# Optimization experiments

Hardware: AMD Instinct MI355X
Metric: run time of the kernel (lower is better)

The kernel has to match this reference:

```python
import jax, jax.numpy as jnp
import numpy as np
from jax import lax

B, T_IN, T_AR = 512, 200, 200
H = 128
L = 2    # num_layers


def setup_inputs() -> dict:
    key = jax.random.key(0)
    k = jax.random.split(key, 8)
    s = 1.0 / np.sqrt(H)
    x = jax.random.normal(k[0], (B, T_IN, H), jnp.float32)
    lengths_in = jax.random.randint(k[1], (B,), T_IN // 2, T_IN + 1).astype(jnp.int32).at[0].set(T_IN)
    lengths_aureg = jax.random.randint(k[2], (B,), T_AR // 2, T_AR + 1).astype(jnp.int32).at[0].set(T_AR)
    mask_aureg = jnp.arange(T_AR)[None, :] < lengths_aureg[:, None]  # [B, T_ar] prefix mask
    W_ih = jax.random.uniform(k[3], (L, 4 * H, H), jnp.float32, -s, s)
    W_hh = jax.random.uniform(k[4], (L, 4 * H, H), jnp.float32, -s, s)
    b_ih = jax.random.uniform(k[5], (L, 4 * H), jnp.float32, -s, s)
    b_hh = jax.random.uniform(k[6], (L, 4 * H), jnp.float32, -s, s)
    return {"x": x, "lengths_in": lengths_in, "lengths_aureg": lengths_aureg,
            "mask_aureg": mask_aureg, "W_ih": W_ih, "W_hh": W_hh, "b_ih": b_ih, "b_hh": b_hh}


def _forward(x, lengths_in, mask_aureg, W_ih, W_hh, b_ih, b_hh):
    def cell_stack(x_t, h, c):
        # one LSTM time step through all layers. x_t: [B,H]; h,c: [L,B,H]
        inp = x_t
        hs, cs = [], []
        for l in range(L):
            z = inp @ W_ih[l].T + h[l] @ W_hh[l].T + (b_ih[l] + b_hh[l])
            i, f, g, o = jnp.split(z, 4, axis=-1)  # PyTorch gate order i,f,g,o
            c_new = jax.nn.sigmoid(f) * c[l] + jax.nn.sigmoid(i) * jnp.tanh(g)
            h_new = jax.nn.sigmoid(o) * jnp.tanh(c_new)
            hs.append(h_new)
            cs.append(c_new)
            inp = h_new
        return jnp.stack(hs), jnp.stack(cs)

    T_in = x.shape[1]
    mask_in = jnp.arange(T_in)[None, :] < lengths_in[:, None]  # [B, T_in]
    h0 = jnp.zeros((L, B, H), x.dtype)

    # Teacher-forcing pass == packed-sequence LSTM: states only advance where t < length,
    # padded output positions are zero (as pad_packed_sequence produces).
    def tf_step(carry, xs):
        h, c = carry
        x_t, m_t = xs  # [B,H], [B]
        h_new, c_new = cell_stack(x_t, h, c)
        m3 = m_t[None, :, None]
        h = jnp.where(m3, h_new, h)
        c = jnp.where(m3, c_new, c)
        out = jnp.where(m_t[:, None], h_new[-1], 0.0)
        return (h, c), out

    (h, c), outs_tf = lax.scan(tf_step, (h0, h0), (x.transpose(1, 0, 2), mask_in.T))
    outputs_teafo = outs_tf.transpose(1, 0, 2)  # [B, T_in, H]

    # input_aureg_init: last-layer hidden at each sequence's final real step
    x_init = h[-1]  # [B, H]

    def ar_step(carry, m_t):
        h, c, xp = carry
        h_new, c_new = cell_stack(xp, h, c)
        m3 = m_t[None, :, None]
        h = jnp.where(m3, h_new, h)
        c = jnp.where(m3, c_new, c)
        out = jnp.where(m_t[:, None], h_new[-1], 0.0)  # temp_output (zeros for inactive rows)
        return (h, c, out), out

    _, outs_ar = lax.scan(ar_step, (h, c, x_init), mask_aureg.T)
    outputs_aureg = outs_ar.transpose(1, 0, 2)  # [B, T_ar, H]
    return outputs_teafo, outputs_aureg


def reference(x, lengths_in, lengths_aureg, mask_aureg, W_ih, W_hh, b_ih, b_hh):
    return _forward(x, lengths_in, mask_aureg, W_ih, W_hh, b_ih, b_hh)
```

## Files before the change

kernel.cpp:

```cpp
#include <hip/hip_runtime.h>
#include <hip/hip_fp16.h>

typedef _Float16 half8 __attribute__((ext_vector_type(8)));
typedef _Float16 half4v __attribute__((ext_vector_type(4)));
typedef float f32x4 __attribute__((ext_vector_type(4)));

#define T_INS 200

constexpr int WI0O = 0;
constexpr int H0O  = 131072;
constexpr int H1O  = 139264;
constexpr int XTO  = 147456;
constexpr int BIO  = 155648;
constexpr int SMSZ = 159744;

constexpr size_t WSZ_PACK = 524288;

#define OFF(b, k) (((((b) << 8) | ((k) << 1))) ^ (((b) & 7) << 4))

#define BARRIER() asm volatile("s_waitcnt lgkmcnt(0)\n\ts_barrier" ::: "memory")

__device__ __forceinline__ float sigm(float x) {
  return __builtin_amdgcn_rcpf(1.0f + __builtin_amdgcn_exp2f(-1.44269504f * x));
}
__device__ __forceinline__ float tanh_f(float x) {
  return 1.0f - 2.0f * __builtin_amdgcn_rcpf(1.0f + __builtin_amdgcn_exp2f(2.88539008f * x));
}
__device__ __forceinline__ half8 cvt_frag(const float* __restrict__ src) {
  f32x4 a = *(const f32x4*)src;
  f32x4 b = *(const f32x4*)(src + 4);
  half8 h;
  h[0] = (_Float16)a[0]; h[1] = (_Float16)a[1]; h[2] = (_Float16)a[2]; h[3] = (_Float16)a[3];
  h[4] = (_Float16)b[0]; h[5] = (_Float16)b[1]; h[6] = (_Float16)b[2]; h[7] = (_Float16)b[3];
  return h;
}
__device__ __forceinline__ half8 cvt_frag_s(const float* __restrict__ src, float s) {
  f32x4 a = *(const f32x4*)src;
  f32x4 b = *(const f32x4*)(src + 4);
  half8 h;
  h[0] = (_Float16)(s * a[0]); h[1] = (_Float16)(s * a[1]);
  h[2] = (_Float16)(s * a[2]); h[3] = (_Float16)(s * a[3]);
  h[4] = (_Float16)(s * b[0]); h[5] = (_Float16)(s * b[1]);
  h[6] = (_Float16)(s * b[2]); h[7] = (_Float16)(s * b[3]);
  return h;
}
__device__ __forceinline__ int perm_row8(int w, int mt, int r) {
  return (r & 3) * 128 + w * 16 + (r >> 2) * 4 + mt;
}

template <int SCALED>
__device__ __forceinline__ float gates(const f32x4 a, float& c, bool mk) {
  float si, sf, tg, so;
  if (SCALED) {
    si = __builtin_amdgcn_rcpf(1.0f + __builtin_amdgcn_exp2f(a[0]));
    sf = __builtin_amdgcn_rcpf(1.0f + __builtin_amdgcn_exp2f(a[1]));
    tg = 1.0f - 2.0f * __builtin_amdgcn_rcpf(1.0f + __builtin_amdgcn_exp2f(a[2]));
    so = __builtin_amdgcn_rcpf(1.0f + __builtin_amdgcn_exp2f(a[3]));
  } else {
    si = sigm(a[0]); sf = sigm(a[1]); tg = tanh_f(a[2]); so = sigm(a[3]);
  }
  float cn = sf * c + si * tg;
  float hn = so * tanh_f(cn);
  c = mk ? cn : c;
  return hn;
}

__global__ __launch_bounds__(256) void pack_kernel(const float* __restrict__ W_ih,
                                                   const float* __restrict__ W_hh,
                                                   char* __restrict__ ws) {
  int gid = blockIdx.x * 256 + threadIdx.x;
  int G = gid >> 6, lane = gid & 63;
  int region = G >> 7, F = G & 127;
  int w = F >> 4, mt = (F >> 2) & 3, kf = F & 3;
  int r = lane & 15;
  int row = perm_row8(w, mt, r);
  int k0 = kf * 32 + (lane >> 4) * 8;
  float s = ((r & 3) == 2) ? 2.88539008f : -1.44269504f;
  const float* src;
  if (region == 0)      src = W_ih + (size_t)(512 + row) * 128 + k0;
  else if (region == 3) src = W_ih + (size_t)row * 128 + k0;
  else                  src = W_hh + (size_t)((region - 1) * 512 + row) * 128 + k0;
  *(half8*)(ws + (size_t)G * 1024 + lane * 16) = cvt_frag_s(src, s);
}

template <int PACKED>
__global__ __launch_bounds__(512, 2) void lstm_kernel(
    const float* __restrict__ x, const int* __restrict__ len_in,
    const int* __restrict__ len_ar, const float* __restrict__ W_ih,
    const float* __restrict__ W_hh, const float* __restrict__ b_ih,
    const float* __restrict__ b_hh, const char* __restrict__ ws,
    float* __restrict__ out) {
  __shared__ __attribute__((aligned(16))) char sm[SMSZ];
  float* biasS = (float*)(sm + BIO);

  const int tid = threadIdx.x;
  const int w = tid >> 6, lane = tid & 63;
  const int lb = lane & 15, lg = lane >> 4;
  const int k0b = lg * 8;
  const int u0 = w * 16 + lg * 4;
  const int batch = blockIdx.x * 16 + lb;
  const int Lin = len_in[batch];
  const int Lar = len_ar[batch];

  if (PACKED) {
    for (int j = 0; j < 16; ++j) {
      int pos = j * 8192 + tid * 16;
      *(half8*)(sm + WI0O + pos) = *(const half8*)(ws + 393216 + pos);
    }
  } else {
    for (int j = 0; j < 16; ++j) {
      int pos = tid * 256 + j * 16;
      int F = pos >> 10, ln = (pos >> 4) & 63;
      int fw = F >> 4, fmt = (F >> 2) & 3, fkf = F & 3;
      int row = perm_row8(fw, fmt, ln & 15);
      int k0 = fkf * 32 + (ln >> 4) * 8;
      *(half8*)(sm + WI0O + pos) = cvt_frag(W_ih + (size_t)row * 128 + k0);
    }
  }
  for (int i = tid; i < 1024; i += 512) {
    int l = i >> 9, rp = i & 511, u = rp >> 2, q = rp & 3;
    float s = PACKED ? ((q == 2) ? 2.88539008f : -1.44269504f) : 1.0f;
    biasS[i] = s * (b_ih[l * 512 + q * 128 + u] + b_hh[l * 512 + q * 128 + u]);
  }
#pragma unroll
  for (int i = 0; i < 2; ++i)
    *(f32x4*)(sm + H0O + tid * 16 + i * 8192) = (f32x4){0.f, 0.f, 0.f, 0.f};
  const int xb = tid >> 5, xk4 = (tid & 31) * 4;
  {
    f32x4 v = *(const f32x4*)(x + ((size_t)(blockIdx.x * 16 + xb) * T_INS) * 128 + xk4);
    half4v hx;
    hx[0] = (_Float16)v[0]; hx[1] = (_Float16)v[1];
    hx[2] = (_Float16)v[2]; hx[3] = (_Float16)v[3];
    *(half4v*)(sm + XTO + OFF(xb, xk4)) = hx;
  }

  half8 whh0[4][4], whh1[4][4], wi1[4][4];
  if (PACKED) {
    const char* base = ws + (size_t)lane * 16;
#pragma unroll
    for (int mt = 0; mt < 4; ++mt)
#pragma unroll
      for (int kf = 0; kf < 4; ++kf) {
        int fo = (w * 16 + mt * 4 + kf) * 1024;
        wi1[mt][kf]  = *(const half8*)(base + fo);
        whh0[mt][kf] = *(const half8*)(base + 131072 + fo);
        whh1[mt][kf] = *(const half8*)(base + 262144 + fo);
      }
  } else {
#pragma unroll
    for (int mt = 0; mt < 4; ++mt)
#pragma unroll
      for (int kf = 0; kf < 4; ++kf) {
        int row = perm_row8(w, mt, lb);
        wi1[mt][kf]  = cvt_frag(W_ih + (size_t)(512 + row) * 128 + kf * 32 + k0b);
        whh0[mt][kf] = cvt_frag(W_hh + (size_t)row * 128 + kf * 32 + k0b);
        whh1[mt][kf] = cvt_frag(W_hh + (size_t)(512 + row) * 128 + kf * 32 + k0b);
      }
  }

  float c0[4], c1[4];
  half4v hp0v, hp1v;
#pragma unroll
  for (int i = 0; i < 4; ++i) {
    c0[i] = c1[i] = 0.f;
    hp0v[i] = (_Float16)0.f; hp1v[i] = (_Float16)0.f;
  }
  __syncthreads();

  const float* xptr = x + ((size_t)(blockIdx.x * 16 + xb) * T_INS + 1) * 128 + xk4;
  float* optr = out + (size_t)batch * 25600 + u0;
  const size_t obase_ar = 13107200ull + (size_t)batch * 25600 + u0;
  const char* wi0base = sm + WI0O + w * 16384 + lane * 16;

  for (int t = 0; t < 400; ++t) {
    const int p = t & 1;
    const bool doX = (t < 199);
    f32x4 xpre = (f32x4){0.f, 0.f, 0.f, 0.f};
    if (doX) { xpre = *(const f32x4*)xptr; xptr += 128; }
    const bool mk = (t < 200) ? (t < Lin) : ((t - 200) < Lar);

    f32x4 acc[4];
    {
      const char* sX = (t < 200) ? (sm + XTO + p * 4096) : (sm + H1O + p * 4096);
      const char* sH = sm + H0O + (p ^ 1) * 4096;
      half8 bf[4];
#pragma unroll
      for (int mt = 0; mt < 4; ++mt)
        acc[mt] = *(const f32x4*)(biasS + (u0 + mt) * 4);
#pragma unroll
      for (int kf = 0; kf < 4; ++kf)
        bf[kf] = *(const half8*)(sH + OFF(lb, kf * 32 + k0b));
#pragma unroll
      for (int kf = 0; kf < 4; ++kf)
#pragma unroll
        for (int mt = 0; mt < 4; ++mt)
          acc[mt] = __builtin_amdgcn_mfma_f32_16x16x32_f16(whh0[mt][kf], bf[kf],
                                                           acc[mt], 0, 0, 0);
#pragma unroll
      for (int kf = 0; kf < 4; ++kf)
        bf[kf] = *(const half8*)(sX + OFF(lb, kf * 32 + k0b));
#pragma unroll
      for (int kf = 0; kf < 4; ++kf)
#pragma unroll
        for (int mt = 0; mt < 4; ++mt) {
          half8 a = *(const half8*)(wi0base + (mt * 4 + kf) * 1024);
          acc[mt] = __builtin_amdgcn_mfma_f32_16x16x32_f16(a, bf[kf], acc[mt], 0, 0, 0);
        }
    }
    {
      _Float16 h4[4];
#pragma unroll
      for (int mt = 0; mt < 4; ++mt)
        h4[mt] = (_Float16)gates<PACKED>(acc[mt], c0[mt], mk);
      hp0v = mk ? *(half4v*)h4 : hp0v;
      *(half4v*)(sm + H0O + p * 4096 + OFF(lb, u0)) = hp0v;
    }
    BARRIER();

    if (doX) {
      half4v hx;
      hx[0] = (_Float16)xpre[0]; hx[1] = (_Float16)xpre[1];
      hx[2] = (_Float16)xpre[2]; hx[3] = (_Float16)xpre[3];
      *(half4v*)(sm + XTO + (p ^ 1) * 4096 + OFF(xb, xk4)) = hx;
    }

    {
      const char* sX = sm + H0O + p * 4096;
      const char* sH = sm + H1O + p * 4096;
      half8 bf[4];
#pragma unroll
      for (int mt = 0; mt < 4; ++mt)
        acc[mt] = *(const f32x4*)(biasS + 512 + (u0 + mt) * 4);
#pragma unroll
      for (int kf = 0; kf < 4; ++kf)
        bf[kf] = *(const half8*)(sH + OFF(lb, kf * 32 + k0b));
#pragma unroll
      for (int kf = 0; kf < 4; ++kf)
#pragma unroll
        for (int mt = 0; mt < 4; ++mt)
          acc[mt] = __builtin_amdgcn_mfma_f32_16x16x32_f16(whh1[mt][kf], bf[kf],
                                                           acc[mt], 0, 0, 0);
#pragma unroll
      for (int kf = 0; kf < 4; ++kf)
        bf[kf] = *(const half8*)(sX + OFF(lb, kf * 32 + k0b));
#pragma unroll
      for (int kf = 0; kf < 4; ++kf)
#pragma unroll
        for (int mt = 0; mt < 4; ++mt)
          acc[mt] = __builtin_amdgcn_mfma_f32_16x16x32_f16(wi1[mt][kf], bf[kf],
                                                           acc[mt], 0, 0, 0);
    }
    {
      _Float16 h4[4];
      f32x4 vo;
#pragma unroll
      for (int mt = 0; mt < 4; ++mt) {
        float hn = gates<PACKED>(acc[mt], c1[mt], mk);
        h4[mt] = (_Float16)hn;
        vo[mt] = mk ? hn : 0.0f;
      }
      hp1v = mk ? *(half4v*)h4 : hp1v;
      *(half4v*)(sm + H1O + (p ^ 1) * 4096 + OFF(lb, u0)) = hp1v;
      *(f32x4*)optr = vo;
      optr += 128;
      if (t == 199) optr = out + obase_ar;
    }
    BARRIER();
  }
}

extern "C" void kernel_launch(void* const* d_in, const int* in_sizes, int n_in,
                              void* d_out, int out_size, void* d_ws, size_t ws_size,
                              hipStream_t stream) {
  (void)in_sizes; (void)n_in; (void)out_size;
  const float* x = (const float*)d_in[0];
  const int* len_in = (const int*)d_in[1];
  const int* len_ar = (const int*)d_in[2];
  const float* W_ih = (const float*)d_in[4];
  const float* W_hh = (const float*)d_in[5];
  const float* b_ih = (const float*)d_in[6];
  const float* b_hh = (const float*)d_in[7];
  float* out = (float*)d_out;
  char* ws = (char*)d_ws;

  if (ws_size >= WSZ_PACK) {
    pack_kernel<<<dim3(128), dim3(256), 0, stream>>>(W_ih, W_hh, ws);
    lstm_kernel<1><<<dim3(32), dim3(512), 0, stream>>>(x, len_in, len_ar, W_ih,
                                                       W_hh, b_ih, b_hh, ws, out);
  } else {
    lstm_kernel<0><<<dim3(32), dim3(512), 0, stream>>>(x, len_in, len_ar, W_ih,
                                                       W_hh, b_ih, b_hh, ws, out);
  }
}
```

Measured before the change: 1.052 ms.

## Split LSTM time loop into phases, prefetch recurrent operands across barriers, keep bias in registers

Splits the 400-step loop into separate teacher-forcing and autoregressive loops, which removes per-step branches on the phase. The recurrent-hidden fragments for the next matmul are now loaded before the barrier (software prefetch), and the barrier waits only for enough LDS ops to retire. Biases move from shared memory into registers and serve as the first MFMA accumulator input. This raises register pressure under the 512-thread, 2-block launch bounds, and the partial lgkmcnt wait must be correct for LDS ordering.

After: 1.604 ms. +52.5%, slower.

```diff
diff --git a/kernel.cpp b/kernel.cpp
--- a/kernel.cpp
+++ b/kernel.cpp
@@ -11,14 +11,13 @@
 constexpr int H0O  = 131072;
 constexpr int H1O  = 139264;
 constexpr int XTO  = 147456;
-constexpr int BIO  = 155648;
-constexpr int SMSZ = 159744;
+constexpr int SMSZ = 155648;
 
 constexpr size_t WSZ_PACK = 524288;
 
 #define OFF(b, k) (((((b) << 8) | ((k) << 1))) ^ (((b) & 7) << 4))
 
-#define BARRIER() asm volatile("s_waitcnt lgkmcnt(0)\n\ts_barrier" ::: "memory")
+#define BAR_K(n) asm volatile("s_waitcnt lgkmcnt(" #n ")\n\ts_barrier" ::: "memory")
 
 __device__ __forceinline__ float sigm(float x) {
   return __builtin_amdgcn_rcpf(1.0f + __builtin_amdgcn_exp2f(-1.44269504f * x));
@@ -83,6 +82,32 @@
   *(half8*)(ws + (size_t)G * 1024 + lane * 16) = cvt_frag_s(src, s);
 }
 
+#define READ_BF(BF, BASE)                                                     \
+  _Pragma("unroll") for (int kf = 0; kf < 4; ++kf)                            \
+      BF[kf] = *(const half8*)((BASE) + OFF(lb, kf * 32 + k0b));
+
+#define MFMA_H(ACC, WREG, BF, BIAS)                                           \
+  _Pragma("unroll") for (int mt = 0; mt < 4; ++mt)                            \
+      ACC[mt] = __builtin_amdgcn_mfma_f32_16x16x32_f16(WREG[mt][0], BF[0],    \
+                                                       BIAS[mt], 0, 0, 0);    \
+  _Pragma("unroll") for (int kf = 1; kf < 4; ++kf)                            \
+      _Pragma("unroll") for (int mt = 0; mt < 4; ++mt)                        \
+          ACC[mt] = __builtin_amdgcn_mfma_f32_16x16x32_f16(WREG[mt][kf],      \
+                                                           BF[kf], ACC[mt], 0, 0, 0);
+
+#define MFMA_X(ACC, WREG, BF)                                                 \
+  _Pragma("unroll") for (int kf = 0; kf < 4; ++kf)                            \
+      _Pragma("unroll") for (int mt = 0; mt < 4; ++mt)                        \
+          ACC[mt] = __builtin_amdgcn_mfma_f32_16x16x32_f16(WREG[mt][kf],      \
+                                                           BF[kf], ACC[mt], 0, 0, 0);
+
+#define MFMA_WI0(ACC, BF)                                                     \
+  _Pragma("unroll") for (int kf = 0; kf < 4; ++kf)                            \
+      _Pragma("unroll") for (int mt = 0; mt < 4; ++mt) {                      \
+        half8 a_ = *(const half8*)(wi0base + (mt * 4 + kf) * 1024);           \
+        ACC[mt] = __builtin_amdgcn_mfma_f32_16x16x32_f16(a_, BF[kf], ACC[mt], 0, 0, 0); \
+      }
+
 template <int PACKED>
 __global__ __launch_bounds__(512, 2) void lstm_kernel(
     const float* __restrict__ x, const int* __restrict__ len_in,
@@ -91,7 +116,6 @@
     const float* __restrict__ b_hh, const char* __restrict__ ws,
     float* __restrict__ out) {
   __shared__ __attribute__((aligned(16))) char sm[SMSZ];
-  float* biasS = (float*)(sm + BIO);
 
   const int tid = threadIdx.x;
   const int w = tid >> 6, lane = tid & 63;
@@ -116,11 +140,6 @@
       int k0 = fkf * 32 + (ln >> 4) * 8;
       *(half8*)(sm + WI0O + pos) = cvt_frag(W_ih + (size_t)row * 128 + k0);
     }
-  }
-  for (int i = tid; i < 1024; i += 512) {
-    int l = i >> 9, rp = i & 511, u = rp >> 2, q = rp & 3;
-    float s = PACKED ? ((q == 2) ? 2.88539008f : -1.44269504f) : 1.0f;
-    biasS[i] = s * (b_ih[l * 512 + q * 128 + u] + b_hh[l * 512 + q * 128 + u]);
   }
 #pragma unroll
   for (int i = 0; i < 2; ++i)
@@ -134,6 +153,18 @@
     *(half4v*)(sm + XTO + OFF(xb, xk4)) = hx;
   }
 
+  f32x4 bias0[4], bias1[4];
+#pragma unroll
+  for (int mt = 0; mt < 4; ++mt) {
+    int u = u0 + mt;
+#pragma unroll
+    for (int q = 0; q < 4; ++q) {
+      float s = PACKED ? ((q == 2) ? 2.88539008f : -1.44269504f) : 1.0f;
+      bias0[mt][q] = s * (b_ih[q * 128 + u] + b_hh[q * 128 + u]);
+      bias1[mt][q] = s * (b_ih[512 + q * 128 + u] + b_hh[512 + q * 128 + u]);
+    }
+  }
+
   half8 whh0[4][4], whh1[4][4], wi1[4][4];
   if (PACKED) {
     const char* base = ws + (size_t)lane * 16;
@@ -167,46 +198,25 @@
   }
   __syncthreads();
 
+  const char* wi0base = sm + WI0O + w * 16384 + lane * 16;
   const float* xptr = x + ((size_t)(blockIdx.x * 16 + xb) * T_INS + 1) * 128 + xk4;
   float* optr = out + (size_t)batch * 25600 + u0;
   const size_t obase_ar = 13107200ull + (size_t)batch * 25600 + u0;
-  const char* wi0base = sm + WI0O + w * 16384 + lane * 16;
-
-  for (int t = 0; t < 400; ++t) {
+
+  f32x4 acc[4];
+  half8 bfA[4], bfB[4];
+  READ_BF(bfA, sm + H0O + 4096);
+
+  for (int t = 0; t < 200; ++t) {
     const int p = t & 1;
     const bool doX = (t < 199);
     f32x4 xpre = (f32x4){0.f, 0.f, 0.f, 0.f};
     if (doX) { xpre = *(const f32x4*)xptr; xptr += 128; }
-    const bool mk = (t < 200) ? (t < Lin) : ((t - 200) < Lar);
-
-    f32x4 acc[4];
-    {
-      const char* sX = (t < 200) ? (sm + XTO + p * 4096) : (sm + H1O + p * 4096);
-      const char* sH = sm + H0O + (p ^ 1) * 4096;
-      half8 bf[4];
-#pragma unroll
-      for (int mt = 0; mt < 4; ++mt)
-        acc[mt] = *(const f32x4*)(biasS + (u0 + mt) * 4);
-#pragma unroll
-      for (int kf = 0; kf < 4; ++kf)
-        bf[kf] = *(const half8*)(sH + OFF(lb, kf * 32 + k0b));
-#pragma unroll
-      for (int kf = 0; kf < 4; ++kf)
-#pragma unroll
-        for (int mt = 0; mt < 4; ++mt)
-          acc[mt] = __builtin_amdgcn_mfma_f32_16x16x32_f16(whh0[mt][kf], bf[kf],
-                                                           acc[mt], 0, 0, 0);
-#pragma unroll
-      for (int kf = 0; kf < 4; ++kf)
-        bf[kf] = *(const half8*)(sX + OFF(lb, kf * 32 + k0b));
-#pragma unroll
-      for (int kf = 0; kf < 4; ++kf)
-#pragma unroll
-        for (int mt = 0; mt < 4; ++mt) {
-          half8 a = *(const half8*)(wi0base + (mt * 4 + kf) * 1024);
-          acc[mt] = __builtin_amdgcn_mfma_f32_16x16x32_f16(a, bf[kf], acc[mt], 0, 0, 0);
-        }
-    }
+    const bool mk = t < Lin;
+
+    MFMA_H(acc, whh0, bfA, bias0);
+    READ_BF(bfB, sm + XTO + p * 4096);
+    MFMA_WI0(acc, bfB);
     {
       _Float16 h4[4];
 #pragma unroll
@@ -215,7 +225,8 @@
       hp0v = mk ? *(half4v*)h4 : hp0v;
       *(half4v*)(sm + H0O + p * 4096 + OFF(lb, u0)) = hp0v;
     }
-    BARRIER();
+    READ_BF(bfB, sm + H1O + p * 4096);
+    BAR_K(4);
 
     if (doX) {
       half4v hx;
@@ -224,32 +235,9 @@
       *(half4v*)(sm + XTO + (p ^ 1) * 4096 + OFF(xb, xk4)) = hx;
     }
 
-    {
-      const char* sX = sm + H0O + p * 4096;
-      const char* sH = sm + H1O + p * 4096;
-      half8 bf[4];
-#pragma unroll
-      for (int mt = 0; mt < 4; ++mt)
-        acc[mt] = *(const f32x4*)(biasS + 512 + (u0 + mt) * 4);
-#pragma unroll
-      for (int kf = 0; kf < 4; ++kf)
-        bf[kf] = *(const half8*)(sH + OFF(lb, kf * 32 + k0b));
-#pragma unroll
-      for (int kf = 0; kf < 4; ++kf)
-#pragma unroll
-        for (int mt = 0; mt < 4; ++mt)
-          acc[mt] = __builtin_amdgcn_mfma_f32_16x16x32_f16(whh1[mt][kf], bf[kf],
-                                                           acc[mt], 0, 0, 0);
-#pragma unroll
-      for (int kf = 0; kf < 4; ++kf)
-        bf[kf] = *(const half8*)(sX + OFF(lb, kf * 32 + k0b));
-#pragma unroll
-      for (int kf = 0; kf < 4; ++kf)
-#pragma unroll
-        for (int mt = 0; mt < 4; ++mt)
-          acc[mt] = __builtin_amdgcn_mfma_f32_16x16x32_f16(wi1[mt][kf], bf[kf],
-                                                           acc[mt], 0, 0, 0);
-    }
+    MFMA_H(acc, whh1, bfB, bias1);
+    READ_BF(bfA, sm + H0O + p * 4096);
+    MFMA_X(acc, wi1, bfA);
     {
       _Float16 h4[4];
       f32x4 vo;
@@ -263,9 +251,46 @@
       *(half4v*)(sm + H1O + (p ^ 1) * 4096 + OFF(lb, u0)) = hp1v;
       *(f32x4*)optr = vo;
       optr += 128;
-      if (t == 199) optr = out + obase_ar;
-    }
-    BARRIER();
+    }
+    BAR_K(0);
+  }
+  optr = out + obase_ar;
+
+  for (int t = 200; t < 400; ++t) {
+    const int p = t & 1;
+    const bool mk = (t - 200) < Lar;
+
+    MFMA_H(acc, whh0, bfA, bias0);
+    READ_BF(bfB, sm + H1O + p * 4096);
+    MFMA_WI0(acc, bfB);
+    {
+      _Float16 h4[4];
+#pragma unroll
+      for (int mt = 0; mt < 4; ++mt)
+        h4[mt] = (_Float16)gates<PACKED>(acc[mt], c0[mt], mk);
+      hp0v = mk ? *(half4v*)h4 : hp0v;
+      *(half4v*)(sm + H0O + p * 4096 + OFF(lb, u0)) = hp0v;
+    }
+    BAR_K(0);
+
+    MFMA_H(acc, whh1, bfB, bias1);
+    READ_BF(bfA, sm + H0O + p * 4096);
+    MFMA_X(acc, wi1, bfA);
+    {
+      _Float16 h4[4];
+      f32x4 vo;
+#pragma unroll
+      for (int mt = 0; mt < 4; ++mt) {
+        float hn = gates<PACKED>(acc[mt], c1[mt], mk);
+        h4[mt] = (_Float16)hn;
+        vo[mt] = mk ? hn : 0.0f;
+      }
+      hp1v = mk ? *(half4v*)h4 : hp1v;
+      *(half4v*)(sm + H1O + (p ^ 1) * 4096 + OFF(lb, u0)) = hp1v;
+      *(f32x4*)optr = vo;
+      optr += 128;
+    }
+    BAR_K(0);
   }
 }
 
```

## Split each block's gate work across 16 waves instead of 8

Applied to the files above, without the earlier changes.

Doubles the workgroup to 1024 threads, so each wave handles 2 M-tiles of the gate matrix instead of 4. This halves the MFMA chain and gate math each wave runs per step on the serial recurrence critical path. The weight packing permutation, register weight fragments and per-lane state are narrowed to match. In exchange, each block now synchronises twice as many waves at every barrier, and every wave still reloads the full B-fragments from LDS, so LDS read traffic goes up.

Result: slower. 1.855 ms (+76.3%).

```diff
diff --git a/kernel.cpp b/kernel.cpp
--- a/kernel.cpp
+++ b/kernel.cpp
@@ -2,8 +2,9 @@
 #include <hip/hip_fp16.h>
 
 typedef _Float16 half8 __attribute__((ext_vector_type(8)));
-typedef _Float16 half4v __attribute__((ext_vector_type(4)));
+typedef _Float16 half2v __attribute__((ext_vector_type(2)));
 typedef float f32x4 __attribute__((ext_vector_type(4)));
+typedef float f32x2 __attribute__((ext_vector_type(2)));
 
 #define T_INS 200
 
@@ -44,8 +45,8 @@
   h[6] = (_Float16)(s * b[2]); h[7] = (_Float16)(s * b[3]);
   return h;
 }
-__device__ __forceinline__ int perm_row8(int w, int mt, int r) {
-  return (r & 3) * 128 + w * 16 + (r >> 2) * 4 + mt;
+__device__ __forceinline__ int perm_row16(int w, int mt, int r) {
+  return (r & 3) * 128 + w * 8 + (r >> 2) * 2 + mt;
 }
 
 template <int SCALED>
@@ -71,9 +72,9 @@
   int gid = blockIdx.x * 256 + threadIdx.x;
   int G = gid >> 6, lane = gid & 63;
   int region = G >> 7, F = G & 127;
-  int w = F >> 4, mt = (F >> 2) & 3, kf = F & 3;
+  int w = F >> 3, mt = (F >> 2) & 1, kf = F & 3;
   int r = lane & 15;
-  int row = perm_row8(w, mt, r);
+  int row = perm_row16(w, mt, r);
   int k0 = kf * 32 + (lane >> 4) * 8;
   float s = ((r & 3) == 2) ? 2.88539008f : -1.44269504f;
   const float* src;
@@ -83,8 +84,12 @@
   *(half8*)(ws + (size_t)G * 1024 + lane * 16) = cvt_frag_s(src, s);
 }
 
+#define READ_BF(BF, BASE)                                                     \
+  _Pragma("unroll") for (int kf = 0; kf < 4; ++kf)                            \
+      BF[kf] = *(const half8*)((BASE) + OFF(lb, kf * 32 + k0b));
+
 template <int PACKED>
-__global__ __launch_bounds__(512, 2) void lstm_kernel(
+__global__ __launch_bounds__(1024, 4) void lstm_kernel(
     const float* __restrict__ x, const int* __restrict__ len_in,
     const int* __restrict__ len_ar, const float* __restrict__ W_ih,
     const float* __restrict__ W_hh, const float* __restrict__ b_ih,
@@ -97,131 +102,124 @@
   const int w = tid >> 6, lane = tid & 63;
   const int lb = lane & 15, lg = lane >> 4;
   const int k0b = lg * 8;
-  const int u0 = w * 16 + lg * 4;
+  const int u0 = w * 8 + lg * 2;
   const int batch = blockIdx.x * 16 + lb;
   const int Lin = len_in[batch];
   const int Lar = len_ar[batch];
 
   if (PACKED) {
-    for (int j = 0; j < 16; ++j) {
-      int pos = j * 8192 + tid * 16;
+    for (int j = 0; j < 8; ++j) {
+      int pos = j * 16384 + tid * 16;
       *(half8*)(sm + WI0O + pos) = *(const half8*)(ws + 393216 + pos);
     }
   } else {
-    for (int j = 0; j < 16; ++j) {
-      int pos = tid * 256 + j * 16;
+    for (int j = 0; j < 8; ++j) {
+      int pos = tid * 128 + j * 16;
       int F = pos >> 10, ln = (pos >> 4) & 63;
-      int fw = F >> 4, fmt = (F >> 2) & 3, fkf = F & 3;
-      int row = perm_row8(fw, fmt, ln & 15);
+      int fw = F >> 3, fmt = (F >> 2) & 1, fkf = F & 3;
+      int row = perm_row16(fw, fmt, ln & 15);
       int k0 = fkf * 32 + (ln >> 4) * 8;
       *(half8*)(sm + WI0O + pos) = cvt_frag(W_ih + (size_t)row * 128 + k0);
     }
   }
-  for (int i = tid; i < 1024; i += 512) {
+  {
+    int i = tid;
     int l = i >> 9, rp = i & 511, u = rp >> 2, q = rp & 3;
     float s = PACKED ? ((q == 2) ? 2.88539008f : -1.44269504f) : 1.0f;
     biasS[i] = s * (b_ih[l * 512 + q * 128 + u] + b_hh[l * 512 + q * 128 + u]);
   }
-#pragma unroll
-  for (int i = 0; i < 2; ++i)
-    *(f32x4*)(sm + H0O + tid * 16 + i * 8192) = (f32x4){0.f, 0.f, 0.f, 0.f};
-  const int xb = tid >> 5, xk4 = (tid & 31) * 4;
+  *(f32x4*)(sm + H0O + tid * 16) = (f32x4){0.f, 0.f, 0.f, 0.f};
+  const int xb = tid >> 6, xk2 = (tid & 63) * 2;
   {
-    f32x4 v = *(const f32x4*)(x + ((size_t)(blockIdx.x * 16 + xb) * T_INS) * 128 + xk4);
-    half4v hx;
+    f32x2 v = *(const f32x2*)(x + ((size_t)(blockIdx.x * 16 + xb) * T_INS) * 128 + xk2);
+    half2v hx;
     hx[0] = (_Float16)v[0]; hx[1] = (_Float16)v[1];
-    hx[2] = (_Float16)v[2]; hx[3] = (_Float16)v[3];
-    *(half4v*)(sm + XTO + OFF(xb, xk4)) = hx;
-  }
-
-  half8 whh0[4][4], whh1[4][4], wi1[4][4];
+    *(half2v*)(sm + XTO + OFF(xb, xk2)) = hx;
+  }
+
+  half8 whh0[2][4], whh1[2][4], wi1[2][4];
   if (PACKED) {
     const char* base = ws + (size_t)lane * 16;
 #pragma unroll
-    for (int mt = 0; mt < 4; ++mt)
+    for (int mt = 0; mt < 2; ++mt)
 #pragma unroll
       for (int kf = 0; kf < 4; ++kf) {
-        int fo = (w * 16 + mt * 4 + kf) * 1024;
+        int fo = (w * 8 + mt * 4 + kf) * 1024;
         wi1[mt][kf]  = *(const half8*)(base + fo);
         whh0[mt][kf] = *(const half8*)(base + 131072 + fo);
         whh1[mt][kf] = *(const half8*)(base + 262144 + fo);
       }
   } else {
 #pragma unroll
-    for (int mt = 0; mt < 4; ++mt)
+    for (int mt = 0; mt < 2; ++mt)
 #pragma unroll
       for (int kf = 0; kf < 4; ++kf) {
-        int row = perm_row8(w, mt, lb);
+        int row = perm_row16(w, mt, lb);
         wi1[mt][kf]  = cvt_frag(W_ih + (size_t)(512 + row) * 128 + kf * 32 + k0b);
         whh0[mt][kf] = cvt_frag(W_hh + (size_t)row * 128 + kf * 32 + k0b);
         whh1[mt][kf] = cvt_frag(W_hh + (size_t)(512 + row) * 128 + kf * 32 + k0b);
       }
   }
 
-  float c0[4], c1[4];
-  half4v hp0v, hp1v;
-#pragma unroll
-  for (int i = 0; i < 4; ++i) {
+  float c0[2], c1[2];
+  half2v hp0v, hp1v;
+#pragma unroll
+  for (int i = 0; i < 2; ++i) {
     c0[i] = c1[i] = 0.f;
     hp0v[i] = (_Float16)0.f; hp1v[i] = (_Float16)0.f;
   }
   __syncthreads();
 
-  const float* xptr = x + ((size_t)(blockIdx.x * 16 + xb) * T_INS + 1) * 128 + xk4;
+  const float* xptr = x + ((size_t)(blockIdx.x * 16 + xb) * T_INS + 1) * 128 + xk2;
   float* optr = out + (size_t)batch * 25600 + u0;
   const size_t obase_ar = 13107200ull + (size_t)batch * 25600 + u0;
-  const char* wi0base = sm + WI0O + w * 16384 + lane * 16;
+  const char* wi0base = sm + WI0O + w * 8192 + lane * 16;
 
   for (int t = 0; t < 400; ++t) {
     const int p = t & 1;
     const bool doX = (t < 199);
-    f32x4 xpre = (f32x4){0.f, 0.f, 0.f, 0.f};
-    if (doX) { xpre = *(const f32x4*)xptr; xptr += 128; }
+    f32x2 xpre = (f32x2){0.f, 0.f};
+    if (doX) { xpre = *(const f32x2*)xptr; xptr += 128; }
     const bool mk = (t < 200) ? (t < Lin) : ((t - 200) < Lar);
 
-    f32x4 acc[4];
+    f32x4 acc[2];
     {
       const char* sX = (t < 200) ? (sm + XTO + p * 4096) : (sm + H1O + p * 4096);
       const char* sH = sm + H0O + (p ^ 1) * 4096;
       half8 bf[4];
 #pragma unroll
-      for (int mt = 0; mt < 4; ++mt)
+      for (int mt = 0; mt < 2; ++mt)
         acc[mt] = *(const f32x4*)(biasS + (u0 + mt) * 4);
-#pragma unroll
-      for (int kf = 0; kf < 4; ++kf)
-        bf[kf] = *(const half8*)(sH + OFF(lb, kf * 32 + k0b));
-#pragma unroll
-      for (int kf = 0; kf < 4; ++kf)
-#pragma unroll
-        for (int mt = 0; mt < 4; ++mt)
+      READ_BF(bf, sH);
+#pragma unroll
+      for (int kf = 0; kf < 4; ++kf)
+#pragma unroll
+        for (int mt = 0; mt < 2; ++mt)
           acc[mt] = __builtin_amdgcn_mfma_f32_16x16x32_f16(whh0[mt][kf], bf[kf],
                                                            acc[mt], 0, 0, 0);
-#pragma unroll
-      for (int kf = 0; kf < 4; ++kf)
-        bf[kf] = *(const half8*)(sX + OFF(lb, kf * 32 + k0b));
-#pragma unroll
-      for (int kf = 0; kf < 4; ++kf)
-#pragma unroll
-        for (int mt = 0; mt < 4; ++mt) {
+      READ_BF(bf, sX);
+#pragma unroll
+      for (int kf = 0; kf < 4; ++kf)
+#pragma unroll
+        for (int mt = 0; mt < 2; ++mt) {
           half8 a = *(const half8*)(wi0base + (mt * 4 + kf) * 1024);
           acc[mt] = __builtin_amdgcn_mfma_f32_16x16x32_f16(a, bf[kf], acc[mt], 0, 0, 0);
         }
     }
     {
-      _Float16 h4[4];
-#pragma unroll
-      for (int mt = 0; mt < 4; ++mt)
-        h4[mt] = (_Float16)gates<PACKED>(acc[mt], c0[mt], mk);
-      hp0v = mk ? *(half4v*)h4 : hp0v;
-      *(half4v*)(sm + H0O + p * 4096 + OFF(lb, u0)) = hp0v;
+      _Float16 h2[2];
+#pragma unroll
+      for (int mt = 0; mt < 2; ++mt)
+        h2[mt] = (_Float16)gates<PACKED>(acc[mt], c0[mt], mk);
+      hp0v = mk ? *(half2v*)h2 : hp0v;
+      *(half2v*)(sm + H0O + p * 4096 + OFF(lb, u0)) = hp0v;
     }
     BARRIER();
 
     if (doX) {
-      half4v hx;
+      half2v hx;
       hx[0] = (_Float16)xpre[0]; hx[1] = (_Float16)xpre[1];
-      hx[2] = (_Float16)xpre[2]; hx[3] = (_Float16)xpre[3];
-      *(half4v*)(sm + XTO + (p ^ 1) * 4096 + OFF(xb, xk4)) = hx;
+      *(half2v*)(sm + XTO + (p ^ 1) * 4096 + OFF(xb, xk2)) = hx;
     }
 
     {
@@ -229,39 +227,35 @@
       const char* sH = sm + H1O + p * 4096;
       half8 bf[4];
 #pragma unroll
-      for (int mt = 0; mt < 4; ++mt)
+      for (int mt = 0; mt < 2; ++mt)
         acc[mt] = *(const f32x4*)(biasS + 512 + (u0 + mt) * 4);
-#pragma unroll
-      for (int kf = 0; kf < 4; ++kf)
-        bf[kf] = *(const half8*)(sH + OFF(lb, kf * 32 + k0b));
-#pragma unroll
-      for (int kf = 0; kf < 4; ++kf)
-#pragma unroll
-        for (int mt = 0; mt < 4; ++mt)
+      READ_BF(bf, sH);
+#pragma unroll
+      for (int kf = 0; kf < 4; ++kf)
+#pragma unroll
+        for (int mt = 0; mt < 2; ++mt)
           acc[mt] = __builtin_amdgcn_mfma_f32_16x16x32_f16(whh1[mt][kf], bf[kf],
                                                            acc[mt], 0, 0, 0);
-#pragma unroll
-      for (int kf = 0; kf < 4; ++kf)
-        bf[kf] = *(const half8*)(sX + OFF(lb, kf * 32 + k0b));
-#pragma unroll
-      for (int kf = 0; kf < 4; ++kf)
-#pragma unroll
-        for (int mt = 0; mt < 4; ++mt)
+      READ_BF(bf, sX);
+#pragma unroll
+      for (int kf = 0; kf < 4; ++kf)
+#pragma unroll
+        for (int mt = 0; mt < 2; ++mt)
           acc[mt] = __builtin_amdgcn_mfma_f32_16x16x32_f16(wi1[mt][kf], bf[kf],
                                                            acc[mt], 0, 0, 0);
     }
     {
-      _Float16 h4[4];
-      f32x4 vo;
-#pragma unroll
-      for (int mt = 0; mt < 4; ++mt) {
+      _Float16 h2[2];
+      f32x2 vo;
+#pragma unroll
+      for (int mt = 0; mt < 2; ++mt) {
         float hn = gates<PACKED>(acc[mt], c1[mt], mk);
-        h4[mt] = (_Float16)hn;
+        h2[mt] = (_Float16)hn;
         vo[mt] = mk ? hn : 0.0f;
       }
-      hp1v = mk ? *(half4v*)h4 : hp1v;
-      *(half4v*)(sm + H1O + (p ^ 1) * 4096 + OFF(lb, u0)) = hp1v;
-      *(f32x4*)optr = vo;
+      hp1v = mk ? *(half2v*)h2 : hp1v;
+      *(half2v*)(sm + H1O + (p ^ 1) * 4096 + OFF(lb, u0)) = hp1v;
+      *(f32x2*)optr = vo;
       optr += 128;
       if (t == 199) optr = out + obase_ar;
     }
@@ -285,10 +279,10 @@
 
   if (ws_size >= WSZ_PACK) {
     pack_kernel<<<dim3(128), dim3(256), 0, stream>>>(W_ih, W_hh, ws);
-    lstm_kernel<1><<<dim3(32), dim3(512), 0, stream>>>(x, len_in, len_ar, W_ih,
-                                                       W_hh, b_ih, b_hh, ws, out);
-  } else {
-    lstm_kernel<0><<<dim3(32), dim3(512), 0, stream>>>(x, len_in, len_ar, W_ih,
-                                                       W_hh, b_ih, b_hh, ws, out);
-  }
-}
+    lstm_kernel<1><<<dim3(32), dim3(1024), 0, stream>>>(x, len_in, len_ar, W_ih,
+                                                        W_hh, b_ih, b_hh, ws, out);
+  } else {
+    lstm_kernel<0><<<dim3(32), dim3(1024), 0, stream>>>(x, len_in, len_ar, W_ih,
+                                                        W_hh, b_ih, b_hh, ws, out);
+  }
+}
```
